# Kernel optimization log

Measured on AMD Instinct MI355X. Metric: run time of the kernel, lower is better.

The kernel has to match this reference:

```python
import jax, jax.numpy as jnp
import numpy as np

DIM = 1024
HEADS = 16
DIM_HEAD = 64
SOFTCAP = 50.0


def setup_inputs() -> dict:
    key = jax.random.key(0)
    k1, k2, k3, k4 = jax.random.split(key, 4)
    b, n = 2, 2048
    dim_inner = HEADS * DIM_HEAD
    x = jax.random.normal(k1, (b, n, DIM), dtype=jnp.float32)
    # parameters stored as math-orientation matrices (in_features, out_features)
    w_qkv = jax.random.normal(k2, (DIM, 3 * dim_inner), dtype=jnp.float32) * 0.02
    w_gates = jax.random.normal(k3, (DIM, HEADS), dtype=jnp.float32) * 0.02
    w_out = jax.random.normal(k4, (dim_inner, DIM), dtype=jnp.float32) * 0.02
    return {"x": x, "w_qkv": w_qkv, "w_gates": w_gates, "w_out": w_out}


def reference(x, w_qkv, w_gates, w_out):
    b, n, _ = x.shape
    scale = DIM_HEAD ** -0.5
    qkv = jnp.einsum('bnf,fe->bne', x, w_qkv).reshape(b, n, 3, HEADS, DIM_HEAD)
    qkv = jnp.moveaxis(qkv, 2, 0)            # 3 b n h d
    q, k, v = jnp.moveaxis(qkv, 3, 2)         # each: b h n d
    q = q * scale
    sim = jnp.einsum('bhid,bhjd->bhij', q, k)
    # tanh softcap on raw scores
    sim = SOFTCAP * jnp.tanh(sim / SOFTCAP)
    # causal mask (prefill path, causal=True)
    mask_value = -jnp.finfo(sim.dtype).max
    causal_mask = jnp.triu(jnp.ones((n, n), dtype=bool), 1)
    sim = jnp.where(causal_mask, mask_value, sim)
    attn = jax.nn.softmax(sim, axis=-1)
    out = jnp.einsum('bhij,bhjd->bhid', attn, v)
    # value gating: sigmoid(x @ Wg) -> b h n 1
    gates = jax.nn.sigmoid(jnp.einsum('bnf,fh->bhn', x, w_gates))[..., None]
    out = out * gates
    # b h n d -> b n (h d) -> output projection
    out = jnp.transpose(out, (0, 2, 1, 3)).reshape(b, n, HEADS * DIM_HEAD)
    return jnp.einsum('bne,ef->bnf', out, w_out)
```

## Files before the change

### kernel.cpp

```cpp
#include <hip/hip_runtime.h>
#include <hip/hip_bf16.h>

typedef __bf16 bf16x8 __attribute__((ext_vector_type(8)));
typedef float f32x4 __attribute__((ext_vector_type(4)));

__device__ __forceinline__ unsigned short f2b(float f) {
    union { float f; unsigned int u; } v; v.f = f;
    unsigned int r = (v.u + 0x7FFFu + ((v.u >> 16) & 1u)) >> 16;
    return (unsigned short)r;
}

__device__ __forceinline__ unsigned int cvtpk(float lo, float hi) {
    unsigned int r;
    asm("v_cvt_pk_bf16_f32 %0, %1, %2" : "=v"(r) : "v"(lo), "v"(hi));
    return r;
}

__device__ __forceinline__ void gload_lds16(const void* g, void* l) {
    __builtin_amdgcn_global_load_lds((__attribute__((address_space(1))) void*)g,
                                     (__attribute__((address_space(3))) void*)l,
                                     16, 0, 0);
}


__global__ __launch_bounds__(256)
void prepass_kernel(const float* __restrict__ x, const float* __restrict__ wg,
                    const float* __restrict__ wq, const float* __restrict__ wo,
                    unsigned short* __restrict__ xb,
                    unsigned short* __restrict__ outq, unsigned short* __restrict__ outo,
                    unsigned short* __restrict__ wgT) {
    __shared__ float tt[32][33];
    const int t = threadIdx.x;
    if (blockIdx.x < 2048) {
        size_t idx = ((size_t)blockIdx.x * 256 + t) * 8;
        float4 f0 = *(const float4*)(x + idx);
        float4 f1 = *(const float4*)(x + idx + 4);
        ushort4 u0, u1;
        u0.x = f2b(f0.x); u0.y = f2b(f0.y); u0.z = f2b(f0.z); u0.w = f2b(f0.w);
        u1.x = f2b(f1.x); u1.y = f2b(f1.y); u1.z = f2b(f1.z); u1.w = f2b(f1.w);
        *(ushort4*)(xb + idx) = u0;
        *(ushort4*)(xb + idx + 4) = u1;
    } else if (blockIdx.x < 6144) {
        const int bx = blockIdx.x - 2048;
        const int colTile = bx & 127;
        const int r0 = (bx >> 7) * 32;
        const float* in;
        unsigned short* out;
        int C, c0;
        if (colTile < 96) { in = wq; out = outq; C = 3072; c0 = colTile * 32; }
        else              { in = wo; out = outo; C = 1024; c0 = (colTile - 96) * 32; }
        const int tx = t & 31, ty = t >> 5;
#pragma unroll
        for (int i = 0; i < 4; i++)
            tt[ty + i * 8][tx] = in[(size_t)(r0 + ty + i * 8) * C + c0 + tx];
        __syncthreads();
#pragma unroll
        for (int i = 0; i < 4; i++)
            out[(size_t)(c0 + ty + i * 8) * 1024 + r0 + tx] = f2b(tt[tx][ty + i * 8]);
    } else {
        const int local = blockIdx.x - 6144;
        const int base = local * 4096 + t * 16;
        const int f = base >> 4;
#pragma unroll
        for (int j = 0; j < 16; j++)
            wgT[j * 1024 + f] = f2b(wg[base + j]);
    }
}


__global__ __launch_bounds__(256)
void gates_mfma_kernel(const unsigned short* __restrict__ xb,
                       const unsigned short* __restrict__ wgT,
                       float* __restrict__ gates) {
    __shared__ float comb[4][16][16];
    const int lane = threadIdx.x & 63;
    const int w = threadIdx.x >> 6;
    const int ql = lane & 15;
    const int g = lane >> 4;
    const int n0 = blockIdx.x * 16;

    f32x4 acc = (f32x4){0.f, 0.f, 0.f, 0.f};
    const int kb = w * 256;
#pragma unroll
    for (int kk = 0; kk < 256; kk += 32) {
        bf16x8 a = *(const bf16x8*)(wgT + ql * 1024 + kb + kk + g * 8);
        bf16x8 bfr = *(const bf16x8*)(xb + (size_t)(n0 + ql) * 1024 + kb + kk + g * 8);
        acc = __builtin_amdgcn_mfma_f32_16x16x32_bf16(a, bfr, acc, 0, 0, 0);
    }
#pragma unroll
    for (int r = 0; r < 4; r++) comb[w][g * 4 + r][ql] = acc[r];
    __syncthreads();
    if (w == 0) {
        const float LOG2E = 1.4426950408889634f;
        int row = n0 + ql;
        int b = row >> 11, n = row & 2047;
#pragma unroll
        for (int r = 0; r < 4; r++) {
            int h = g * 4 + r;
            float tot = comb[0][h][ql] + comb[1][h][ql] + comb[2][h][ql] + comb[3][h][ql];
            float sg = __builtin_amdgcn_rcpf(1.f + __builtin_amdgcn_exp2f(-tot * LOG2E));
            gates[((size_t)(b * 16 + h)) * 2048 + n] = sg;
        }
    }
}


template <int EPI, int WN>
__global__ __launch_bounds__(256)
void gemm_bt_kernel(const unsigned short* __restrict__ A,
                    const unsigned short* __restrict__ Bt,
                    int M, int N, int K,
                    unsigned short* __restrict__ outQ,
                    unsigned short* __restrict__ outK,
                    unsigned short* __restrict__ outV,
                    float* __restrict__ outF) {
    constexpr int WM = 4 / WN;
    constexpr int MF = 8 / WM;
    constexpr int BN = 64 * WN;
    __shared__ unsigned short As[2][128 * 32];
    __shared__ unsigned short Bs[2][BN * 32];
    const int lane = threadIdx.x & 63;
    const int w = threadIdx.x >> 6;
    const int wr = w / WN, wc = w % WN;
    const int tm = blockIdx.y * 128;
    const int tn = blockIdx.x * BN;

    f32x4 acc[MF][4];
#pragma unroll
    for (int m = 0; m < MF; m++)
#pragma unroll
        for (int n = 0; n < 4; n++) acc[m][n] = (f32x4){0.f, 0.f, 0.f, 0.f};

    const int sRow = lane >> 2;
    const int sCol = (lane & 3) * 8;
    const int fragA = (wr * (16 * MF) + (lane & 15)) * 32 + (lane >> 4) * 8;
    const int fragB = (wc * 64 + (lane & 15)) * 32 + (lane >> 4) * 8;

    auto STAGE = [&](int k0, int buf) {
#pragma unroll
        for (int i = 0; i < 2; i++) {
            int chunk = w * 2 + i;
            int r = chunk * 16 + sRow;
            gload_lds16(A + (size_t)(tm + r) * K + k0 + sCol, (void*)(As[buf] + chunk * 512));
            if (WN == 2)
                gload_lds16(Bt + (size_t)(tn + r) * K + k0 + sCol, (void*)(Bs[buf] + chunk * 512));
        }
        if (WN == 1) {
            int r = w * 16 + sRow;
            gload_lds16(Bt + (size_t)(tn + r) * K + k0 + sCol, (void*)(Bs[buf] + w * 512));
        }
    };

    STAGE(0, 0);
    __syncthreads();
    int cur = 0;
    for (int k0 = 0; k0 < K; k0 += 32) {
        if (k0 + 32 < K) STAGE(k0 + 32, cur ^ 1);
        bf16x8 af[MF], bg[4];
#pragma unroll
        for (int m = 0; m < MF; m++) af[m] = *(const bf16x8*)(As[cur] + fragA + m * 16 * 32);
#pragma unroll
        for (int n = 0; n < 4; n++) bg[n] = *(const bf16x8*)(Bs[cur] + fragB + n * 16 * 32);
#pragma unroll
        for (int m = 0; m < MF; m++)
#pragma unroll
            for (int n = 0; n < 4; n++)
                acc[m][n] = __builtin_amdgcn_mfma_f32_16x16x32_bf16(af[m], bg[n], acc[m][n], 0, 0, 0);
        __syncthreads();
        cur ^= 1;
    }

#pragma unroll
    for (int m = 0; m < MF; m++) {
        int row = tm + wr * (16 * MF) + m * 16 + (lane >> 4) * 4;
#pragma unroll
        for (int n = 0; n < 4; n++) {
            int col = tn + wc * 64 + n * 16 + (lane & 15);
            if (EPI == 0) {
                int which = col >> 10;
                int hh = (col >> 6) & 15;
                int d = col & 63;
                int b0 = row >> 11;
                int nn = row & 2047;
                size_t bh = (size_t)(b0 * 16 + hh);
                if (which == 2) {
                    int i6 = nn & 63;
                    int pc = (nn & ~63) + ((i6 >> 2) & 3) * 16 + ((i6 >> 4) & 3) * 4;
                    ushort4 st;
                    st.x = f2b(acc[m][n][0]);
                    st.y = f2b(acc[m][n][1]);
                    st.z = f2b(acc[m][n][2]);
                    st.w = f2b(acc[m][n][3]);
                    *(ushort4*)(outV + bh * 131072 + (size_t)d * 2048 + pc) = st;
                } else if (which == 0) {
                    size_t off = (bh * 2048 + nn) * 64 + d;
#pragma unroll
                    for (int r = 0; r < 4; r++)
                        outQ[off + (size_t)r * 64] = f2b(acc[m][n][r] * 0.125f);
                } else {
                    size_t off = (bh * 2048 + nn) * 64 + d;
#pragma unroll
                    for (int r = 0; r < 4; r++)
                        outK[off + (size_t)r * 64] = f2b(acc[m][n][r]);
                }
            } else {
#pragma unroll
                for (int r = 0; r < 4; r++)
                    outF[(size_t)(row + r) * N + col] = acc[m][n][r];
            }
        }
    }
}


__global__ __launch_bounds__(256)
void attn_kernel(const unsigned short* __restrict__ Q,
                 const unsigned short* __restrict__ Kg,
                 const unsigned short* __restrict__ Vp,
                 const float* __restrict__ Gates,
                 unsigned short* __restrict__ Out) {
    __shared__ unsigned short lds[2][2][2][64][64];

    const int lane = threadIdx.x & 63;
    const int w = threadIdx.x >> 6;
    const int g = lane >> 4;
    const int ql = lane & 15;
    const int sw = ql & 7;
    const int srow = lane >> 3;
    const int sch = lane & 7;

    const int wgid = (blockIdx.x & 7) * 64 + (blockIdx.x >> 3);
    const int bh = wgid >> 4;
    const int pair = wgid & 15;
    const int b = bh >> 4;
    const int h = bh & 15;

    const size_t headBase = (size_t)bh * 2048 * 64;
    const size_t vBase = (size_t)bh * 131072;

    const int koff0 = ((g) ^ sw) * 8;
    const int koff1 = ((g + 4) ^ sw) * 8;
    const int voff0 = ((2 * g) ^ sw) * 8;
    const int voff1 = ((2 * g + 1) ^ sw) * 8;

    const int ch = sch ^ srow;
    const unsigned short* kSt0 = Kg + headBase + (size_t)(w * 16 + srow) * 64 + ch * 8;
    const unsigned short* kSt1 = kSt0 + 8 * 64;
    const unsigned short* vSt0 = Vp + vBase + (size_t)(w * 16 + srow) * 2048 + ch * 8;
    const unsigned short* vSt1 = vSt0 + 8 * 2048;

    auto STAGE = [&](int jn, int buf, int slot) {
        gload_lds16(kSt0 + (size_t)jn * 4096, (void*)&lds[buf][slot][0][w * 16][0]);
        gload_lds16(kSt1 + (size_t)jn * 4096, (void*)&lds[buf][slot][0][w * 16 + 8][0]);
        gload_lds16(vSt0 + jn * 64, (void*)&lds[buf][slot][1][w * 16][0]);
        gload_lds16(vSt1 + jn * 64, (void*)&lds[buf][slot][1][w * 16 + 8][0]);
    };

    const float LOG2E = 1.4426950408889634f;
    const float LC1 = -1.9235933878519511e-4f;
    const float LC2 = 3.0777494205631219e-8f;

    for (int half = 0; half < 2; half++) {
        const int qt = half ? (31 - pair) : pair;
        const int qglob = qt * 64 + w * 16 + ql;
        const int T = qt + 1;
        const int nPairs = (T + 1) >> 1;

        const unsigned short* qp = Q + headBase + (size_t)qglob * 64 + g * 8;
        bf16x8 qa0 = *(const bf16x8*)qp;
        bf16x8 qa1 = *(const bf16x8*)(qp + 32);

        float lsum = 0.f;
        f32x4 o[4];
#pragma unroll
        for (int n = 0; n < 4; n++) o[n] = (f32x4){0.f, 0.f, 0.f, 0.f};

        auto COMPUTE = [&](int jt, int bb, int slot, bool diag) {
            const unsigned short* KL = &lds[bb][slot][0][0][0];
            const unsigned short* VL = &lds[bb][slot][1][0][0];

            f32x4 s4[4];
            __builtin_amdgcn_s_setprio(1);
#pragma unroll
            for (int n = 0; n < 4; n++) {
                const unsigned short* kr = KL + (16 * n + ql) * 64;
                bf16x8 k0 = *(const bf16x8*)(kr + koff0);
                bf16x8 k1 = *(const bf16x8*)(kr + koff1);
                f32x4 sv = (f32x4){0.f, 0.f, 0.f, 0.f};
                sv = __builtin_amdgcn_mfma_f32_16x16x32_bf16(k0, qa0, sv, 0, 0, 0);
                sv = __builtin_amdgcn_mfma_f32_16x16x32_bf16(k1, qa1, sv, 0, 0, 0);
                s4[n] = sv;
            }
            __builtin_amdgcn_s_setprio(0);

            float rs = 0.f;
#pragma unroll
            for (int n = 0; n < 4; n++) {
                int k0c = jt * 64 + n * 16 + 4 * g;
#pragma unroll
                for (int r = 0; r < 4; r++) {
                    float xx = s4[n][r];
                    float x2 = xx * xx;
                    float e2 = xx * __builtin_fmaf(x2, __builtin_fmaf(x2, LC2, LC1), LOG2E);
                    if (diag && (k0c + r > qglob)) e2 = -1e30f;
                    float p = __builtin_amdgcn_exp2f(e2);
                    s4[n][r] = p;
                    rs += p;
                }
            }
            lsum += rs;

            union PU { unsigned int u[4]; bf16x8 v; };
            PU p0, p1;
            p0.u[0] = cvtpk(s4[0][0], s4[0][1]);
            p0.u[1] = cvtpk(s4[0][2], s4[0][3]);
            p0.u[2] = cvtpk(s4[1][0], s4[1][1]);
            p0.u[3] = cvtpk(s4[1][2], s4[1][3]);
            p1.u[0] = cvtpk(s4[2][0], s4[2][1]);
            p1.u[1] = cvtpk(s4[2][2], s4[2][3]);
            p1.u[2] = cvtpk(s4[3][0], s4[3][1]);
            p1.u[3] = cvtpk(s4[3][2], s4[3][3]);

            __builtin_amdgcn_s_setprio(1);
#pragma unroll
            for (int n = 0; n < 4; n++) {
                const unsigned short* vr = VL + (16 * n + ql) * 64;
                bf16x8 vA = *(const bf16x8*)(vr + voff0);
                bf16x8 vB = *(const bf16x8*)(vr + voff1);
                o[n] = __builtin_amdgcn_mfma_f32_16x16x32_bf16(vA, p0.v, o[n], 0, 0, 0);
                o[n] = __builtin_amdgcn_mfma_f32_16x16x32_bf16(vB, p1.v, o[n], 0, 0, 0);
            }
            __builtin_amdgcn_s_setprio(0);
        };

        STAGE(0, 0, 0);
        if (1 <= qt) STAGE(1, 0, 1);
        __syncthreads();

        for (int p = 0; p < nPairs - 1; ++p) {
            const int bb = p & 1;
            const int j2 = 2 * (p + 1);
            STAGE(j2, bb ^ 1, 0);
            if (j2 + 1 <= qt) STAGE(j2 + 1, bb ^ 1, 1);
            COMPUTE(2 * p, bb, 0, false);
            COMPUTE(2 * p + 1, bb, 1, false);
            __syncthreads();
        }
        {
            const int p = nPairs - 1;
            const int bb = p & 1;
            COMPUTE(2 * p, bb, 0, 2 * p == qt);
            if (2 * p + 1 <= qt) COMPUTE(2 * p + 1, bb, 1, true);
            __syncthreads();
        }

        float l = lsum;
        l += __shfl_xor(l, 16);
        l += __shfl_xor(l, 32);
        float gate = Gates[(size_t)bh * 2048 + qglob];
        float inv = gate / l;
        unsigned short* orow = Out + ((size_t)(b * 2048) + qglob) * 1024 + h * 64;
#pragma unroll
        for (int n = 0; n < 4; n++) {
            ushort4 st;
            st.x = f2b(o[n][0] * inv);
            st.y = f2b(o[n][1] * inv);
            st.z = f2b(o[n][2] * inv);
            st.w = f2b(o[n][3] * inv);
            *(ushort4*)(orow + n * 16 + 4 * g) = st;
        }
    }
}


extern "C" void kernel_launch(void* const* d_in, const int* in_sizes, int n_in,
                              void* d_out, int out_size, void* d_ws, size_t ws_size,
                              hipStream_t stream) {
    const float* x       = (const float*)d_in[0];
    const float* w_qkv   = (const float*)d_in[1];
    const float* w_gates = (const float*)d_in[2];
    const float* w_out   = (const float*)d_in[3];
    float* out = (float*)d_out;

    char* ws = (char*)d_ws;
    unsigned short* x_bf  = (unsigned short*)(ws);
    unsigned short* wqkvT = (unsigned short*)(ws + ((size_t)8  << 20));
    unsigned short* woutT = (unsigned short*)(ws + ((size_t)14 << 20));
    unsigned short* qB    = (unsigned short*)(ws + ((size_t)16 << 20));
    unsigned short* kB    = (unsigned short*)(ws + ((size_t)24 << 20));
    unsigned short* vP    = (unsigned short*)(ws + ((size_t)32 << 20));
    float*          gates = (float*)(ws + ((size_t)40 << 20));
    unsigned short* wgT   = (unsigned short*)(ws + ((size_t)40 << 20) + (512 << 10));
    unsigned short* attnO = (unsigned short*)(ws + ((size_t)41 << 20));

    prepass_kernel<<<dim3(6148), dim3(256), 0, stream>>>(
        x, w_gates, w_qkv, w_out, x_bf, wqkvT, woutT, wgT);

    gates_mfma_kernel<<<dim3(256), dim3(256), 0, stream>>>(x_bf, wgT, gates);

    gemm_bt_kernel<0, 2><<<dim3(3072 / 128, 4096 / 128), dim3(256), 0, stream>>>(
        x_bf, wqkvT, 4096, 3072, 1024, qB, kB, vP, (float*)nullptr);

    attn_kernel<<<dim3(512), dim3(256), 0, stream>>>(qB, kB, vP, gates, attnO);

    gemm_bt_kernel<1, 1><<<dim3(1024 / 64, 4096 / 128), dim3(256), 0, stream>>>(
        attnO, woutT, 4096, 1024, 1024, nullptr, nullptr, nullptr, out);
}
```

Baseline: 109.5 us.

## Share K/V tiles across two query tiles per 512-thread attention block

The attention kernel now launches 256 blocks of 512 threads instead of 512 blocks of 256. Each half of the block (four waves) handles one of two adjacent query tiles, and both halves share the staged K/V tiles, each loading one of the two KV tiles per step. This halves redundant K/V global loads and LDS staging per query tile. The cost is fewer blocks, barriers spanning twice as many waves, and some idle waves at the causal diagonal, where one tile needs one more KV tile than the other.

```diff
diff --git a/kernel.cpp b/kernel.cpp
--- a/kernel.cpp
+++ b/kernel.cpp
@@ -213,7 +213,7 @@
 }
 
 
-__global__ __launch_bounds__(256)
+__global__ __launch_bounds__(512)
 void attn_kernel(const unsigned short* __restrict__ Q,
                  const unsigned short* __restrict__ Kg,
                  const unsigned short* __restrict__ Vp,
@@ -223,15 +223,17 @@
 
     const int lane = threadIdx.x & 63;
     const int w = threadIdx.x >> 6;
+    const int qw = w & 3;
+    const int wv = w >> 2;
     const int g = lane >> 4;
     const int ql = lane & 15;
     const int sw = ql & 7;
     const int srow = lane >> 3;
     const int sch = lane & 7;
 
-    const int wgid = (blockIdx.x & 7) * 64 + (blockIdx.x >> 3);
-    const int bh = wgid >> 4;
-    const int pair = wgid & 15;
+    const int wgid = (blockIdx.x & 7) * 32 + (blockIdx.x >> 3);
+    const int bh = wgid >> 3;
+    const int tsel = wgid & 7;
     const int b = bh >> 4;
     const int h = bh & 15;
 
@@ -244,27 +246,27 @@
     const int voff1 = ((2 * g + 1) ^ sw) * 8;
 
     const int ch = sch ^ srow;
-    const unsigned short* kSt0 = Kg + headBase + (size_t)(w * 16 + srow) * 64 + ch * 8;
+    const unsigned short* kSt0 = Kg + headBase + (size_t)(qw * 16 + srow) * 64 + ch * 8;
     const unsigned short* kSt1 = kSt0 + 8 * 64;
-    const unsigned short* vSt0 = Vp + vBase + (size_t)(w * 16 + srow) * 2048 + ch * 8;
+    const unsigned short* vSt0 = Vp + vBase + (size_t)(qw * 16 + srow) * 2048 + ch * 8;
     const unsigned short* vSt1 = vSt0 + 8 * 2048;
 
-    auto STAGE = [&](int jn, int buf, int slot) {
-        gload_lds16(kSt0 + (size_t)jn * 4096, (void*)&lds[buf][slot][0][w * 16][0]);
-        gload_lds16(kSt1 + (size_t)jn * 4096, (void*)&lds[buf][slot][0][w * 16 + 8][0]);
-        gload_lds16(vSt0 + jn * 64, (void*)&lds[buf][slot][1][w * 16][0]);
-        gload_lds16(vSt1 + jn * 64, (void*)&lds[buf][slot][1][w * 16 + 8][0]);
+    auto STAGE = [&](int jn, int buf) {
+        gload_lds16(kSt0 + (size_t)jn * 4096, (void*)&lds[buf][wv][0][qw * 16][0]);
+        gload_lds16(kSt1 + (size_t)jn * 4096, (void*)&lds[buf][wv][0][qw * 16 + 8][0]);
+        gload_lds16(vSt0 + jn * 64, (void*)&lds[buf][wv][1][qw * 16][0]);
+        gload_lds16(vSt1 + jn * 64, (void*)&lds[buf][wv][1][qw * 16 + 8][0]);
     };
 
     const float LOG2E = 1.4426950408889634f;
     const float LC1 = -1.9235933878519511e-4f;
     const float LC2 = 3.0777494205631219e-8f;
 
-    for (int half = 0; half < 2; half++) {
-        const int qt = half ? (31 - pair) : pair;
-        const int qglob = qt * 64 + w * 16 + ql;
-        const int T = qt + 1;
-        const int nPairs = (T + 1) >> 1;
+    for (int grp = 0; grp < 2; grp++) {
+        const int B = grp ? (30 - 2 * tsel) : (2 * tsel);
+        const int qt = B + wv;
+        const int qglob = qt * 64 + qw * 16 + ql;
+        const int nP = (B + 2) >> 1;
 
         const unsigned short* qp = Q + headBase + (size_t)qglob * 64 + g * 8;
         bf16x8 qa0 = *(const bf16x8*)qp;
@@ -333,24 +335,23 @@
             __builtin_amdgcn_s_setprio(0);
         };
 
-        STAGE(0, 0, 0);
-        if (1 <= qt) STAGE(1, 0, 1);
+        STAGE(wv, 0);
         __syncthreads();
 
-        for (int p = 0; p < nPairs - 1; ++p) {
+        for (int p = 0; p < nP - 1; ++p) {
             const int bb = p & 1;
-            const int j2 = 2 * (p + 1);
-            STAGE(j2, bb ^ 1, 0);
-            if (j2 + 1 <= qt) STAGE(j2 + 1, bb ^ 1, 1);
-            COMPUTE(2 * p, bb, 0, false);
-            COMPUTE(2 * p + 1, bb, 1, false);
+            STAGE(2 * (p + 1) + wv, bb ^ 1);
+            const int jt0 = 2 * p, jt1 = 2 * p + 1;
+            if (jt0 <= qt) COMPUTE(jt0, bb, 0, jt0 == qt);
+            if (jt1 <= qt) COMPUTE(jt1, bb, 1, jt1 == qt);
             __syncthreads();
         }
         {
-            const int p = nPairs - 1;
+            const int p = nP - 1;
             const int bb = p & 1;
-            COMPUTE(2 * p, bb, 0, 2 * p == qt);
-            if (2 * p + 1 <= qt) COMPUTE(2 * p + 1, bb, 1, true);
+            const int jt0 = 2 * p, jt1 = 2 * p + 1;
+            if (jt0 <= qt) COMPUTE(jt0, bb, 0, jt0 == qt);
+            if (jt1 <= qt) COMPUTE(jt1, bb, 1, jt1 == qt);
             __syncthreads();
         }
 
@@ -401,7 +402,7 @@
     gemm_bt_kernel<0, 2><<<dim3(3072 / 128, 4096 / 128), dim3(256), 0, stream>>>(
         x_bf, wqkvT, 4096, 3072, 1024, qB, kB, vP, (float*)nullptr);
 
-    attn_kernel<<<dim3(512), dim3(256), 0, stream>>>(qB, kB, vP, gates, attnO);
+    attn_kernel<<<dim3(256), dim3(512), 0, stream>>>(qB, kB, vP, gates, attnO);
 
     gemm_bt_kernel<1, 1><<<dim3(1024 / 64, 4096 / 128), dim3(256), 0, stream>>>(
         attnO, woutT, 4096, 1024, 1024, nullptr, nullptr, nullptr, out);
```

After: 110.2 us. No clear change (+0.7%).

## Split attention into one workgroup per query tile with longest-first ordering

Applied to the files above, without the earlier changes.

Each workgroup now handles a single 64-row query tile instead of a balanced pair (qt, 31-qt), so the grid doubles to 1024 blocks. The block-to-tile mapping puts the longest causal tiles first and groups heads per XCD-stride. LDS staging drops from two K/V tiles per stage to one, which halves shared memory and may raise occupancy. In exchange there are twice as many barriers per unit of work and per-block work becomes imbalanced, relying on the scheduler to fill the tail.

```diff
diff --git a/kernel.cpp b/kernel.cpp
--- a/kernel.cpp
+++ b/kernel.cpp
@@ -219,7 +219,7 @@
                  const unsigned short* __restrict__ Vp,
                  const float* __restrict__ Gates,
                  unsigned short* __restrict__ Out) {
-    __shared__ unsigned short lds[2][2][2][64][64];
+    __shared__ unsigned short lds[2][2][64][64];
 
     const int lane = threadIdx.x & 63;
     const int w = threadIdx.x >> 6;
@@ -229,9 +229,12 @@
     const int srow = lane >> 3;
     const int sch = lane & 7;
 
-    const int wgid = (blockIdx.x & 7) * 64 + (blockIdx.x >> 3);
-    const int bh = wgid >> 4;
-    const int pair = wgid & 15;
+    const int x = blockIdx.x & 7;
+    const int c = (blockIdx.x >> 3) & 31;
+    const int j = blockIdx.x >> 8;
+    const int bh = x * 4 + (c & 3);
+    const int s = c >> 2;
+    const int qt = (j == 0) ? (31 - s) : (j == 1) ? s : (j == 2) ? (23 - s) : (8 + s);
     const int b = bh >> 4;
     const int h = bh & 15;
 
@@ -249,126 +252,110 @@
     const unsigned short* vSt0 = Vp + vBase + (size_t)(w * 16 + srow) * 2048 + ch * 8;
     const unsigned short* vSt1 = vSt0 + 8 * 2048;
 
-    auto STAGE = [&](int jn, int buf, int slot) {
-        gload_lds16(kSt0 + (size_t)jn * 4096, (void*)&lds[buf][slot][0][w * 16][0]);
-        gload_lds16(kSt1 + (size_t)jn * 4096, (void*)&lds[buf][slot][0][w * 16 + 8][0]);
-        gload_lds16(vSt0 + jn * 64, (void*)&lds[buf][slot][1][w * 16][0]);
-        gload_lds16(vSt1 + jn * 64, (void*)&lds[buf][slot][1][w * 16 + 8][0]);
+    auto STAGE = [&](int jn, int buf) {
+        gload_lds16(kSt0 + (size_t)jn * 4096, (void*)&lds[buf][0][w * 16][0]);
+        gload_lds16(kSt1 + (size_t)jn * 4096, (void*)&lds[buf][0][w * 16 + 8][0]);
+        gload_lds16(vSt0 + jn * 64, (void*)&lds[buf][1][w * 16][0]);
+        gload_lds16(vSt1 + jn * 64, (void*)&lds[buf][1][w * 16 + 8][0]);
     };
 
     const float LOG2E = 1.4426950408889634f;
     const float LC1 = -1.9235933878519511e-4f;
     const float LC2 = 3.0777494205631219e-8f;
 
-    for (int half = 0; half < 2; half++) {
-        const int qt = half ? (31 - pair) : pair;
-        const int qglob = qt * 64 + w * 16 + ql;
-        const int T = qt + 1;
-        const int nPairs = (T + 1) >> 1;
-
-        const unsigned short* qp = Q + headBase + (size_t)qglob * 64 + g * 8;
-        bf16x8 qa0 = *(const bf16x8*)qp;
-        bf16x8 qa1 = *(const bf16x8*)(qp + 32);
-
-        float lsum = 0.f;
-        f32x4 o[4];
-#pragma unroll
-        for (int n = 0; n < 4; n++) o[n] = (f32x4){0.f, 0.f, 0.f, 0.f};
-
-        auto COMPUTE = [&](int jt, int bb, int slot, bool diag) {
-            const unsigned short* KL = &lds[bb][slot][0][0][0];
-            const unsigned short* VL = &lds[bb][slot][1][0][0];
-
-            f32x4 s4[4];
-            __builtin_amdgcn_s_setprio(1);
-#pragma unroll
-            for (int n = 0; n < 4; n++) {
-                const unsigned short* kr = KL + (16 * n + ql) * 64;
-                bf16x8 k0 = *(const bf16x8*)(kr + koff0);
-                bf16x8 k1 = *(const bf16x8*)(kr + koff1);
-                f32x4 sv = (f32x4){0.f, 0.f, 0.f, 0.f};
-                sv = __builtin_amdgcn_mfma_f32_16x16x32_bf16(k0, qa0, sv, 0, 0, 0);
-                sv = __builtin_amdgcn_mfma_f32_16x16x32_bf16(k1, qa1, sv, 0, 0, 0);
-                s4[n] = sv;
+    const int qglob = qt * 64 + w * 16 + ql;
+    const unsigned short* qp = Q + headBase + (size_t)qglob * 64 + g * 8;
+    bf16x8 qa0 = *(const bf16x8*)qp;
+    bf16x8 qa1 = *(const bf16x8*)(qp + 32);
+
+    float lsum = 0.f;
+    f32x4 o[4];
+#pragma unroll
+    for (int n = 0; n < 4; n++) o[n] = (f32x4){0.f, 0.f, 0.f, 0.f};
+
+    auto COMPUTE = [&](int jt, int bb, bool diag) {
+        const unsigned short* KL = &lds[bb][0][0][0];
+        const unsigned short* VL = &lds[bb][1][0][0];
+
+        f32x4 s4[4];
+        __builtin_amdgcn_s_setprio(1);
+#pragma unroll
+        for (int n = 0; n < 4; n++) {
+            const unsigned short* kr = KL + (16 * n + ql) * 64;
+            bf16x8 k0 = *(const bf16x8*)(kr + koff0);
+            bf16x8 k1 = *(const bf16x8*)(kr + koff1);
+            f32x4 sv = (f32x4){0.f, 0.f, 0.f, 0.f};
+            sv = __builtin_amdgcn_mfma_f32_16x16x32_bf16(k0, qa0, sv, 0, 0, 0);
+            sv = __builtin_amdgcn_mfma_f32_16x16x32_bf16(k1, qa1, sv, 0, 0, 0);
+            s4[n] = sv;
+        }
+        __builtin_amdgcn_s_setprio(0);
+
+        float rs = 0.f;
+#pragma unroll
+        for (int n = 0; n < 4; n++) {
+            int k0c = jt * 64 + n * 16 + 4 * g;
+#pragma unroll
+            for (int r = 0; r < 4; r++) {
+                float xx = s4[n][r];
+                float x2 = xx * xx;
+                float e2 = xx * __builtin_fmaf(x2, __builtin_fmaf(x2, LC2, LC1), LOG2E);
+                if (diag && (k0c + r > qglob)) e2 = -1e30f;
+                float p = __builtin_amdgcn_exp2f(e2);
+                s4[n][r] = p;
+                rs += p;
             }
-            __builtin_amdgcn_s_setprio(0);
-
-            float rs = 0.f;
-#pragma unroll
-            for (int n = 0; n < 4; n++) {
-                int k0c = jt * 64 + n * 16 + 4 * g;
-#pragma unroll
-                for (int r = 0; r < 4; r++) {
-                    float xx = s4[n][r];
-                    float x2 = xx * xx;
-                    float e2 = xx * __builtin_fmaf(x2, __builtin_fmaf(x2, LC2, LC1), LOG2E);
-                    if (diag && (k0c + r > qglob)) e2 = -1e30f;
-                    float p = __builtin_amdgcn_exp2f(e2);
-                    s4[n][r] = p;
-                    rs += p;
-                }
-            }
-            lsum += rs;
-
-            union PU { unsigned int u[4]; bf16x8 v; };
-            PU p0, p1;
-            p0.u[0] = cvtpk(s4[0][0], s4[0][1]);
-            p0.u[1] = cvtpk(s4[0][2], s4[0][3]);
-            p0.u[2] = cvtpk(s4[1][0], s4[1][1]);
-            p0.u[3] = cvtpk(s4[1][2], s4[1][3]);
-            p1.u[0] = cvtpk(s4[2][0], s4[2][1]);
-            p1.u[1] = cvtpk(s4[2][2], s4[2][3]);
-            p1.u[2] = cvtpk(s4[3][0], s4[3][1]);
-            p1.u[3] = cvtpk(s4[3][2], s4[3][3]);
-
-            __builtin_amdgcn_s_setprio(1);
-#pragma unroll
-            for (int n = 0; n < 4; n++) {
-                const unsigned short* vr = VL + (16 * n + ql) * 64;
-                bf16x8 vA = *(const bf16x8*)(vr + voff0);
-                bf16x8 vB = *(const bf16x8*)(vr + voff1);
-                o[n] = __builtin_amdgcn_mfma_f32_16x16x32_bf16(vA, p0.v, o[n], 0, 0, 0);
-                o[n] = __builtin_amdgcn_mfma_f32_16x16x32_bf16(vB, p1.v, o[n], 0, 0, 0);
-            }
-            __builtin_amdgcn_s_setprio(0);
-        };
-
-        STAGE(0, 0, 0);
-        if (1 <= qt) STAGE(1, 0, 1);
+        }
+        lsum += rs;
+
+        union PU { unsigned int u[4]; bf16x8 v; };
+        PU p0, p1;
+        p0.u[0] = cvtpk(s4[0][0], s4[0][1]);
+        p0.u[1] = cvtpk(s4[0][2], s4[0][3]);
+        p0.u[2] = cvtpk(s4[1][0], s4[1][1]);
+        p0.u[3] = cvtpk(s4[1][2], s4[1][3]);
+        p1.u[0] = cvtpk(s4[2][0], s4[2][1]);
+        p1.u[1] = cvtpk(s4[2][2], s4[2][3]);
+        p1.u[2] = cvtpk(s4[3][0], s4[3][1]);
+        p1.u[3] = cvtpk(s4[3][2], s4[3][3]);
+
+        __builtin_amdgcn_s_setprio(1);
+#pragma unroll
+        for (int n = 0; n < 4; n++) {
+            const unsigned short* vr = VL + (16 * n + ql) * 64;
+            bf16x8 vA = *(const bf16x8*)(vr + voff0);
+            bf16x8 vB = *(const bf16x8*)(vr + voff1);
+            o[n] = __builtin_amdgcn_mfma_f32_16x16x32_bf16(vA, p0.v, o[n], 0, 0, 0);
+            o[n] = __builtin_amdgcn_mfma_f32_16x16x32_bf16(vB, p1.v, o[n], 0, 0, 0);
+        }
+        __builtin_amdgcn_s_setprio(0);
+    };
+
+    STAGE(0, 0);
+    __syncthreads();
+
+    for (int jt = 0; jt < qt; ++jt) {
+        const int bb = jt & 1;
+        STAGE(jt + 1, bb ^ 1);
+        COMPUTE(jt, bb, false);
         __syncthreads();
-
-        for (int p = 0; p < nPairs - 1; ++p) {
-            const int bb = p & 1;
-            const int j2 = 2 * (p + 1);
-            STAGE(j2, bb ^ 1, 0);
-            if (j2 + 1 <= qt) STAGE(j2 + 1, bb ^ 1, 1);
-            COMPUTE(2 * p, bb, 0, false);
-            COMPUTE(2 * p + 1, bb, 1, false);
-            __syncthreads();
-        }
-        {
-            const int p = nPairs - 1;
-            const int bb = p & 1;
-            COMPUTE(2 * p, bb, 0, 2 * p == qt);
-            if (2 * p + 1 <= qt) COMPUTE(2 * p + 1, bb, 1, true);
-            __syncthreads();
-        }
-
-        float l = lsum;
-        l += __shfl_xor(l, 16);
-        l += __shfl_xor(l, 32);
-        float gate = Gates[(size_t)bh * 2048 + qglob];
-        float inv = gate / l;
-        unsigned short* orow = Out + ((size_t)(b * 2048) + qglob) * 1024 + h * 64;
-#pragma unroll
-        for (int n = 0; n < 4; n++) {
-            ushort4 st;
-            st.x = f2b(o[n][0] * inv);
-            st.y = f2b(o[n][1] * inv);
-            st.z = f2b(o[n][2] * inv);
-            st.w = f2b(o[n][3] * inv);
-            *(ushort4*)(orow + n * 16 + 4 * g) = st;
-        }
+    }
+    COMPUTE(qt, qt & 1, true);
+
+    float l = lsum;
+    l += __shfl_xor(l, 16);
+    l += __shfl_xor(l, 32);
+    float gate = Gates[(size_t)bh * 2048 + qglob];
+    float inv = gate / l;
+    unsigned short* orow = Out + ((size_t)(b * 2048) + qglob) * 1024 + h * 64;
+#pragma unroll
+    for (int n = 0; n < 4; n++) {
+        ushort4 st;
+        st.x = f2b(o[n][0] * inv);
+        st.y = f2b(o[n][1] * inv);
+        st.z = f2b(o[n][2] * inv);
+        st.w = f2b(o[n][3] * inv);
+        *(ushort4*)(orow + n * 16 + 4 * g) = st;
     }
 }
 
@@ -401,7 +388,7 @@
     gemm_bt_kernel<0, 2><<<dim3(3072 / 128, 4096 / 128), dim3(256), 0, stream>>>(
         x_bf, wqkvT, 4096, 3072, 1024, qB, kB, vP, (float*)nullptr);
 
-    attn_kernel<<<dim3(512), dim3(256), 0, stream>>>(qB, kB, vP, gates, attnO);
+    attn_kernel<<<dim3(1024), dim3(256), 0, stream>>>(qB, kB, vP, gates, attnO);
 
     gemm_bt_kernel<1, 1><<<dim3(1024 / 64, 4096 / 128), dim3(256), 0, stream>>>(
         attnO, woutT, 4096, 1024, 1024, nullptr, nullptr, nullptr, out);
```

New measurement: 107.8 us. About the same (-1.6%).
